# Kernel tuning notes

Measured on AMD Instinct MI355X. Metric: run time of the kernel, lower is better.

Reference implementation:

```python
import jax, jax.numpy as jnp
import numpy as np

B, L, C = 16, 450, 768
MID = 256
K = 8912
TEMP = 0.07
ENT_TEMP = 0.01
EPS_NORM = 1e-12


def _l2norm(v):
    n = jnp.sqrt(jnp.sum(v * v, axis=-1, keepdims=True))
    return v / jnp.maximum(n, EPS_NORM)


def setup_inputs() -> dict:
    key = jax.random.key(0)
    k1, k2, k3, k4 = jax.random.split(key, 4)
    x = jax.random.normal(k1, (B, L, C), dtype=jnp.float32)
    W_down = jax.random.normal(k2, (C, MID), dtype=jnp.float32) * (1.0 / np.sqrt(C))
    b_down = jnp.zeros((MID,), dtype=jnp.float32)
    bound = 1.0 / np.sqrt(MID)
    embedding = jax.random.uniform(k3, (K, MID), dtype=jnp.float32, minval=-bound, maxval=bound)
    return {"x": x, "W_down": W_down, "b_down": b_down, "embedding": embedding}


def reference(x, W_down, b_down, embedding):
    Bx, Lx, Cx = x.shape
    # down projection: [B,L,C] -> [B,L,MID]
    z = jnp.einsum('blc,cm->blm', x, W_down) + b_down
    zf = z.reshape(Bx * Lx, MID)
    zn = _l2norm(zf)                       # [N, MID]
    en = _l2norm(embedding)                # [K, MID]
    # squared euclidean distance on the unit sphere: ||a-b||^2 = 2 - 2 a.b
    d = 2.0 - 2.0 * jnp.einsum('nm,km->nk', zn, en)   # [N, K]
    idx = jnp.argmin(d, axis=1)            # [N]
    # codebook usage (no-grad stats)
    occ = jnp.bincount(idx, length=K)
    code_book_usage = jnp.mean((occ > 0).astype(jnp.float32))
    # soft assignment probs (hard_quant branch)
    logits = -d / TEMP
    probs = jax.nn.softmax(logits, axis=1)
    z_q = en[idx]                          # [N, MID]
    vq_loss = jnp.mean((z_q - jax.lax.stop_gradient(zn)) ** 2)
    commit_loss = jnp.mean((jax.lax.stop_gradient(z_q) - zn) ** 2)
    # straight-through estimator
    z_q_ste = zn + jax.lax.stop_gradient(z_q - zn)
    # entropy loss on affinity = -d at entropy temperature
    fa = -d / ENT_TEMP
    p = jax.nn.softmax(fa, axis=-1)
    lp = jax.nn.log_softmax(fa, axis=-1)
    avg_probs = jnp.mean(p, axis=0)
    avg_entropy = -jnp.sum(avg_probs * jnp.log(avg_probs + 1e-5))
    sample_entropy = -jnp.mean(jnp.sum(p * lp, axis=-1))
    entropy_loss = sample_entropy - avg_entropy
    return (z_q_ste.reshape(Bx, Lx, MID), probs.reshape(Bx, Lx, K),
            code_book_usage, vq_loss, commit_loss, entropy_loss)
```

## Files before the change

kernel.cpp:

```cpp
#include <hip/hip_runtime.h>
#include <stdint.h>

#define N_TOK 7200
#define N_PAD 7232
#define N_PAD_A 7296
#define K_CODE 8912
#define K_PAD 8960
#define N_KT 140
#define NKT128 70
#define NMT128 57
#define MID 256
#define C_DIM 768
#define INV_TEMP (1.0f/0.07f)
#define INV_ETEMP 100.0f
#define MARGIN 0.02f
#define CAND_CAP 64
#define EPS_N 1e-12f

typedef __attribute__((ext_vector_type(8))) short short8;
typedef __attribute__((ext_vector_type(4))) float f32x4;

__device__ __forceinline__ unsigned short f2bf(float f) {
    unsigned u = __float_as_uint(f);
    u += 0x7fffu + ((u >> 16) & 1u);
    return (unsigned short)(u >> 16);
}
__device__ __forceinline__ float bf2f(unsigned short h) {
    return __uint_as_float(((unsigned)h) << 16);
}

__device__ __forceinline__ void gload16(const void* g, void* l) {
    __builtin_amdgcn_global_load_lds(
        (const __attribute__((address_space(1))) unsigned int*)g,
        (__attribute__((address_space(3))) unsigned int*)l,
        16, 0, 0);
}

__global__ void k_prep(const float* __restrict__ emb,
                       float* __restrict__ en, unsigned short* __restrict__ en_h,
                       const float* __restrict__ W,
                       unsigned short* __restrict__ wt_h, unsigned short* __restrict__ wt_l,
                       float* __restrict__ ap_acc, int* __restrict__ used,
                       float* __restrict__ acc4, int* __restrict__ ccnt,
                       unsigned short* __restrict__ zn_h) {
    __shared__ float sb[256];
    int b = blockIdx.x, t = threadIdx.x;
    if (b < K_CODE) {
        float v = emb[b * MID + t];
        sb[t] = v * v; __syncthreads();
        for (int s = 128; s > 0; s >>= 1) { if (t < s) sb[t] += sb[t + s]; __syncthreads(); }
        float nn = sqrtf(sb[0]);
        float o = v / fmaxf(nn, EPS_N);
        en[b * MID + t] = o;
        en_h[b * MID + t] = f2bf(o);
    } else if (b < K_CODE + 768) {
        int i = (b - K_CODE) * 256 + t;
        int c = i / MID, tc = i % MID;
        float v = W[i];
        unsigned short h = f2bf(v);
        unsigned short l = f2bf(v - bf2f(h));
        wt_h[tc * C_DIM + c] = h;
        wt_l[tc * C_DIM + c] = l;
    } else {
        int i = (b - K_CODE - 768) * 256 + t;
        if (i < K_CODE) { ap_acc[i] = 0.f; used[i] = 0; }
        if (i < N_TOK) ccnt[i] = 0;
        if (i < 4) acc4[i] = 0.f;
        for (int j = i; j < (N_PAD_A - N_TOK) * MID; j += 8960) zn_h[(size_t)N_TOK * MID + j] = 0;
        for (int j = i; j < (K_PAD - K_CODE) * MID; j += 8960) en_h[(size_t)K_CODE * MID + j] = 0;
    }
}

__global__ __launch_bounds__(256) void k_zgemm(const float* __restrict__ x,
                                               const unsigned short* __restrict__ wt_h,
                                               const unsigned short* __restrict__ wt_l,
                                               float* __restrict__ zbuf) {
    __shared__ unsigned short ls[4 * 64 * 72];
    unsigned short* xh = ls;
    unsigned short* xl = ls + 64 * 72;
    unsigned short* wh = ls + 2 * 64 * 72;
    unsigned short* wl = ls + 3 * 64 * 72;
    int tid = threadIdx.x;
    int m0 = blockIdx.y * 64;
    int t0 = blockIdx.x * 64;
    int lane = tid & 63, wv = tid >> 6;
    int quad = lane >> 4, l15 = lane & 15;
    int mrow0 = (wv >> 1) * 32, ncol0 = (wv & 1) * 32;
    f32x4 acc[2][2] = {};

    for (int ch = 0; ch < 12; ch++) {
        int c0 = ch * 64;
        for (int it = 0; it < 4; it++) {
            int r = it * 16 + (tid >> 4);
            int cq = tid & 15;
            float4 v = make_float4(0.f, 0.f, 0.f, 0.f);
            int gr = m0 + r;
            if (gr < N_TOK) v = ((const float4*)x)[(size_t)gr * (C_DIM / 4) + (c0 >> 2) + cq];
            unsigned short h0 = f2bf(v.x), h1 = f2bf(v.y), h2 = f2bf(v.z), h3 = f2bf(v.w);
            ushort4 hh = make_ushort4(h0, h1, h2, h3);
            ushort4 ll = make_ushort4(f2bf(v.x - bf2f(h0)), f2bf(v.y - bf2f(h1)),
                                      f2bf(v.z - bf2f(h2)), f2bf(v.w - bf2f(h3)));
            *((ushort4*)&xh[r * 72 + cq * 4]) = hh;
            *((ushort4*)&xl[r * 72 + cq * 4]) = ll;
        }
        for (int it = 0; it < 2; it++) {
            int r = it * 32 + (tid >> 3);
            int cq = tid & 7;
            uint4 vh = ((const uint4*)wt_h)[(size_t)(t0 + r) * (C_DIM / 8) + (c0 >> 3) + cq];
            uint4 vl = ((const uint4*)wt_l)[(size_t)(t0 + r) * (C_DIM / 8) + (c0 >> 3) + cq];
            *((uint4*)&wh[r * 72 + cq * 8]) = vh;
            *((uint4*)&wl[r * 72 + cq * 8]) = vl;
        }
        __syncthreads();
        for (int ks = 0; ks < 2; ks++) {
            int co = ks * 32 + quad * 8;
            short8 ah0 = *((const short8*)&xh[(mrow0 + l15) * 72 + co]);
            short8 ah1 = *((const short8*)&xh[(mrow0 + 16 + l15) * 72 + co]);
            short8 al0 = *((const short8*)&xl[(mrow0 + l15) * 72 + co]);
            short8 al1 = *((const short8*)&xl[(mrow0 + 16 + l15) * 72 + co]);
            short8 bh0 = *((const short8*)&wh[(ncol0 + l15) * 72 + co]);
            short8 bh1 = *((const short8*)&wh[(ncol0 + 16 + l15) * 72 + co]);
            short8 bl0 = *((const short8*)&wl[(ncol0 + l15) * 72 + co]);
            short8 bl1 = *((const short8*)&wl[(ncol0 + 16 + l15) * 72 + co]);
            acc[0][0] = __builtin_amdgcn_mfma_f32_16x16x32_bf16(ah0, bh0, acc[0][0], 0, 0, 0);
            acc[0][1] = __builtin_amdgcn_mfma_f32_16x16x32_bf16(ah0, bh1, acc[0][1], 0, 0, 0);
            acc[1][0] = __builtin_amdgcn_mfma_f32_16x16x32_bf16(ah1, bh0, acc[1][0], 0, 0, 0);
            acc[1][1] = __builtin_amdgcn_mfma_f32_16x16x32_bf16(ah1, bh1, acc[1][1], 0, 0, 0);
            acc[0][0] = __builtin_amdgcn_mfma_f32_16x16x32_bf16(ah0, bl0, acc[0][0], 0, 0, 0);
            acc[0][1] = __builtin_amdgcn_mfma_f32_16x16x32_bf16(ah0, bl1, acc[0][1], 0, 0, 0);
            acc[1][0] = __builtin_amdgcn_mfma_f32_16x16x32_bf16(ah1, bl0, acc[1][0], 0, 0, 0);
            acc[1][1] = __builtin_amdgcn_mfma_f32_16x16x32_bf16(ah1, bl1, acc[1][1], 0, 0, 0);
            acc[0][0] = __builtin_amdgcn_mfma_f32_16x16x32_bf16(al0, bh0, acc[0][0], 0, 0, 0);
            acc[0][1] = __builtin_amdgcn_mfma_f32_16x16x32_bf16(al0, bh1, acc[0][1], 0, 0, 0);
            acc[1][0] = __builtin_amdgcn_mfma_f32_16x16x32_bf16(al1, bh0, acc[1][0], 0, 0, 0);
            acc[1][1] = __builtin_amdgcn_mfma_f32_16x16x32_bf16(al1, bh1, acc[1][1], 0, 0, 0);
        }
        __syncthreads();
    }
    for (int i = 0; i < 2; i++)
        for (int j = 0; j < 2; j++)
            for (int r = 0; r < 4; r++) {
                int gr = m0 + mrow0 + i * 16 + quad * 4 + r;
                int gc = t0 + ncol0 + j * 16 + l15;
                if (gr < N_TOK) zbuf[(size_t)gr * MID + gc] = acc[i][j][r];
            }
}

__global__ void k_znorm(float* __restrict__ zbuf, const float* __restrict__ b_down,
                        unsigned short* __restrict__ zn_h) {
    int n = blockIdx.x, t = threadIdx.x;
    float v = zbuf[(size_t)n * MID + t] + b_down[t];
    __shared__ float sb[256];
    sb[t] = v * v; __syncthreads();
    for (int s = 128; s > 0; s >>= 1) { if (t < s) sb[t] += sb[t + s]; __syncthreads(); }
    float nn = sqrtf(sb[0]);
    float o = v / fmaxf(nn, EPS_N);
    zbuf[(size_t)n * MID + t] = o;
    zn_h[(size_t)n * MID + t] = f2bf(o);
}

__global__ __launch_bounds__(256) void k_dgemm(const unsigned short* __restrict__ zn_h,
                                               const unsigned short* __restrict__ en_h,
                                               float4* __restrict__ part4,
                                               float* __restrict__ out1) {
    __shared__ __align__(16) char lds[32768];
    int tid = threadIdx.x;
    int flat = blockIdx.x * NMT128 + blockIdx.y;
    const int NW = NKT128 * NMT128;
    const int q = NW >> 3, r8 = NW & 7;
    int xcd = flat & 7, sidx = flat >> 3;
    int wg = (xcd < r8 ? xcd * (q + 1) : r8 * (q + 1) + (xcd - r8) * q) + sidx;
    int kt = wg / NMT128, mt = wg - kt * NMT128;
    int m0 = mt * 128, k0 = kt * 128;
    int lane = tid & 63, wv = tid >> 6;
    int quad = lane >> 4, l15 = lane & 15;
    int wr = wv >> 1, wc = wv & 1;
    f32x4 acc[4][4] = {};

    int sr = tid >> 3;
    int scb = (tid & 7) * 16;

    for (int step = 0; step < 4; step++) {
        int cB = step * 128;
        #pragma unroll
        for (int it = 0; it < 4; it++) {
            int r = it * 32 + sr;
            int srcb = scb ^ ((r & 7) << 4);
            gload16((const char*)zn_h + (size_t)(m0 + r) * 512 + cB + srcb,
                    lds + it * 4096 + wv * 1024);
            gload16((const char*)en_h + (size_t)(k0 + r) * 512 + cB + srcb,
                    lds + 16384 + it * 4096 + wv * 1024);
        }
        __syncthreads();
        #pragma unroll
        for (int ks = 0; ks < 2; ks++) {
            short8 a[4], b[4];
            #pragma unroll
            for (int i = 0; i < 4; i++) {
                int ra = wr * 64 + i * 16 + l15;
                int ca = (ks * 64 + quad * 16) ^ ((ra & 7) << 4);
                a[i] = *(const short8*)(lds + ra * 128 + ca);
                int rb = wc * 64 + i * 16 + l15;
                int cb2 = (ks * 64 + quad * 16) ^ ((rb & 7) << 4);
                b[i] = *(const short8*)(lds + 16384 + rb * 128 + cb2);
            }
            #pragma unroll
            for (int i = 0; i < 4; i++)
                #pragma unroll
                for (int j = 0; j < 4; j++)
                    acc[i][j] = __builtin_amdgcn_mfma_f32_16x16x32_bf16(a[i], b[j], acc[i][j], 0, 0, 0);
        }
        __syncthreads();
    }

    int kth = kt * 2 + wc;
    #pragma unroll
    for (int i = 0; i < 4; i++) {
        #pragma unroll
        for (int r = 0; r < 4; r++) {
            int gr = m0 + wr * 64 + i * 16 + quad * 4 + r;
            bool okr = gr < N_TOK;
            float dv[4]; float vmin = 1e30f;
            #pragma unroll
            for (int j = 0; j < 4; j++) {
                int gc = k0 + wc * 64 + j * 16 + l15;
                float d = 2.f - 2.f * acc[i][j][r];
                bool okc = gc < K_CODE;
                dv[j] = okc ? d : 1e30f;
                vmin = fminf(vmin, dv[j]);
                if (okr && okc) out1[(size_t)gr * K_CODE + gc] = d;
            }
            vmin = fminf(vmin, __shfl_xor(vmin, 1));
            vmin = fminf(vmin, __shfl_xor(vmin, 2));
            vmin = fminf(vmin, __shfl_xor(vmin, 4));
            vmin = fminf(vmin, __shfl_xor(vmin, 8));
            float st = 0.f, s1 = 0.f, s2 = 0.f;
            #pragma unroll
            for (int j = 0; j < 4; j++) {
                float dd = vmin - dv[j];
                st += __expf(dd * INV_TEMP);
                float te = dd * INV_ETEMP;
                float e = __expf(te);
                s1 += e; s2 += e * te;
            }
            st += __shfl_xor(st, 1); st += __shfl_xor(st, 2);
            st += __shfl_xor(st, 4); st += __shfl_xor(st, 8);
            s1 += __shfl_xor(s1, 1); s1 += __shfl_xor(s1, 2);
            s1 += __shfl_xor(s1, 4); s1 += __shfl_xor(s1, 8);
            s2 += __shfl_xor(s2, 1); s2 += __shfl_xor(s2, 2);
            s2 += __shfl_xor(s2, 4); s2 += __shfl_xor(s2, 8);
            if (l15 == 0 && okr) {
                part4[(size_t)gr * N_KT + kth] = make_float4(vmin, st, s1, s2);
            }
        }
    }
}

__global__ void k_combine(const float4* __restrict__ part4,
                          float* __restrict__ rs_m, float* __restrict__ rs_ist,
                          float* __restrict__ rs_is1,
                          float* __restrict__ acc4) {
    int sub = threadIdx.x >> 6;
    int row = blockIdx.x * 4 + sub;
    int l = threadIdx.x & 63;
    float4 pv[3];
    float m = 1e30f;
    #pragma unroll
    for (int c = 0; c < 3; c++) {
        int t = l + c * 64;
        pv[c] = (t < N_KT) ? part4[(size_t)row * N_KT + t] : make_float4(1e30f, 0.f, 0.f, 0.f);
        m = fminf(m, pv[c].x);
    }
    #pragma unroll
    for (int s = 1; s < 64; s <<= 1) m = fminf(m, __shfl_xor(m, s));
    float st = 0.f, s1 = 0.f, s2 = 0.f;
    #pragma unroll
    for (int c = 0; c < 3; c++) {
        float mb = pv[c].x;
        int t = l + c * 64;
        if (t < N_KT && mb < 1e29f) {
            float dT = (m - mb) * INV_TEMP;
            st += __expf(dT) * pv[c].y;
            float dE = (m - mb) * INV_ETEMP;
            float e = __expf(dE);
            s1 += e * pv[c].z;
            s2 += e * (pv[c].w + dE * pv[c].z);
        }
    }
    #pragma unroll
    for (int s = 1; s < 64; s <<= 1) {
        st += __shfl_xor(st, s);
        s1 += __shfl_xor(s1, s);
        s2 += __shfl_xor(s2, s);
    }
    if (l == 0) {
        rs_m[row] = m;
        rs_ist[row] = 1.f / st;
        rs_is1[row] = 1.f / s1;
        atomicAdd(&acc4[1], s2 / s1 - __logf(s1));
    }
}

__global__ __launch_bounds__(256) void k_final(float* __restrict__ out1,
                                               const float* __restrict__ rs_m,
                                               const float* __restrict__ rs_ist,
                                               const float* __restrict__ rs_is1,
                                               float* __restrict__ ap_acc,
                                               int* __restrict__ ccnt,
                                               int* __restrict__ cand) {
    __shared__ float lm[128], lt_[128], l1_[128];
    __shared__ float colacc[4 * 256];
    int ct = blockIdx.x, rt = blockIdx.y;
    int r0 = rt * 128, c0 = ct * 256;
    int t = threadIdx.x;
    if (t < 128) {
        int gr = r0 + t;
        bool ok = gr < N_TOK;
        lm[t]  = ok ? rs_m[gr]   : 0.f;
        lt_[t] = ok ? rs_ist[gr] : 0.f;
        l1_[t] = ok ? rs_is1[gr] : 0.f;
    }
    __syncthreads();
    int g = t >> 6;
    int cq = (t & 63) * 4;
    int gc = c0 + cq;
    float ce0 = 0.f, ce1 = 0.f, ce2 = 0.f, ce3 = 0.f;
    if (gc < K_CODE) {
        for (int i = 0; i < 32; i++) {
            int lr = g * 32 + i;
            int gr = r0 + lr;
            if (gr >= N_TOK) break;
            size_t base = (size_t)gr * K_CODE + gc;
            float4 d = *(const float4*)(out1 + base);
            float m_ = lm[lr], tt = lt_[lr], i1 = l1_[lr];
            float thr = m_ + MARGIN;
            ce0 += __expf((m_ - d.x) * INV_ETEMP) * i1;
            ce1 += __expf((m_ - d.y) * INV_ETEMP) * i1;
            ce2 += __expf((m_ - d.z) * INV_ETEMP) * i1;
            ce3 += __expf((m_ - d.w) * INV_ETEMP) * i1;
            float4 p;
            p.x = __expf((m_ - d.x) * INV_TEMP) * tt;
            p.y = __expf((m_ - d.y) * INV_TEMP) * tt;
            p.z = __expf((m_ - d.z) * INV_TEMP) * tt;
            p.w = __expf((m_ - d.w) * INV_TEMP) * tt;
            *((float4*)(out1 + base)) = p;
            if (d.x <= thr) { int pd = atomicAdd(&ccnt[gr], 1); if (pd < CAND_CAP) cand[gr * CAND_CAP + pd] = gc + 0; }
            if (d.y <= thr) { int pd = atomicAdd(&ccnt[gr], 1); if (pd < CAND_CAP) cand[gr * CAND_CAP + pd] = gc + 1; }
            if (d.z <= thr) { int pd = atomicAdd(&ccnt[gr], 1); if (pd < CAND_CAP) cand[gr * CAND_CAP + pd] = gc + 2; }
            if (d.w <= thr) { int pd = atomicAdd(&ccnt[gr], 1); if (pd < CAND_CAP) cand[gr * CAND_CAP + pd] = gc + 3; }
        }
    }
    colacc[g * 256 + cq + 0] = ce0;
    colacc[g * 256 + cq + 1] = ce1;
    colacc[g * 256 + cq + 2] = ce2;
    colacc[g * 256 + cq + 3] = ce3;
    __syncthreads();
    {
        float s = colacc[t] + colacc[256 + t] + colacc[512 + t] + colacc[768 + t];
        int c = c0 + t;
        if (c < K_CODE) atomicAdd(&ap_acc[c], s);
    }
}

__global__ void k_refine(const float* __restrict__ zn, const float* __restrict__ en,
                         const int* __restrict__ ccnt, const int* __restrict__ cand,
                         int* __restrict__ idxb, int* __restrict__ used,
                         float* __restrict__ acc4, float* __restrict__ out0) {
    int n = blockIdx.x * 4 + (threadIdx.x >> 6);
    int lane = threadIdx.x & 63;
    if (n >= N_TOK) return;
    int cnt = ccnt[n];
    if (cnt > CAND_CAP) cnt = CAND_CAP;
    float4 a = ((const float4*)(zn + (size_t)n * MID))[lane];
    float best = 1e30f; int bj = K_CODE;
    for (int c = 0; c < cnt; c++) {
        int code = cand[n * CAND_CAP + c];
        float4 b = ((const float4*)(en + (size_t)code * MID))[lane];
        float s = a.x * b.x + a.y * b.y + a.z * b.z + a.w * b.w;
        #pragma unroll
        for (int off = 1; off < 64; off <<= 1) s += __shfl_xor(s, off);
        float dist = 2.f - 2.f * s;
        if (dist < best || (dist == best && code < bj)) { best = dist; bj = code; }
    }
    float4 b = ((const float4*)(en + (size_t)bj * MID))[lane];
    ((float4*)(out0 + (size_t)n * MID))[lane] = b;
    float dx = b.x - a.x, dy = b.y - a.y, dz = b.z - a.z, dw = b.w - a.w;
    float sq = dx * dx + dy * dy + dz * dz + dw * dw;
    #pragma unroll
    for (int off = 32; off > 0; off >>= 1) sq += __shfl_down(sq, off);
    if (lane == 0) {
        idxb[n] = bj;
        used[bj] = 1;
        atomicAdd(&acc4[0], sq);
    }
}

__global__ void k_scal(const int* __restrict__ used, const float* __restrict__ ap_acc,
                       const float* __restrict__ acc4, float* __restrict__ outs) {
    int t = threadIdx.x;
    float uSum = 0.f, aeSum = 0.f;
    for (int k = t; k < K_CODE; k += 256) {
        uSum += (float)used[k];
        float ap = ap_acc[k] * (1.0f / (float)N_TOK);
        aeSum += ap * __logf(ap + 1e-5f);
    }
    __shared__ float sb[256];
    sb[t] = uSum; __syncthreads();
    for (int s = 128; s > 0; s >>= 1) { if (t < s) sb[t] += sb[t + s]; __syncthreads(); }
    uSum = sb[0];
    __syncthreads(); sb[t] = aeSum; __syncthreads();
    for (int s = 128; s > 0; s >>= 1) { if (t < s) sb[t] += sb[t + s]; __syncthreads(); }
    aeSum = sb[0];
    if (t == 0) {
        outs[0] = uSum / (float)K_CODE;
        float vq = acc4[0] / (float)((size_t)N_TOK * MID);
        outs[1] = vq;
        outs[2] = vq;
        outs[3] = -(acc4[1] / (float)N_TOK) + aeSum;
    }
}

extern "C" void kernel_launch(void* const* d_in, const int* in_sizes, int n_in,
                              void* d_out, int out_size, void* d_ws, size_t ws_size,
                              hipStream_t stream) {
    const float* x   = (const float*)d_in[0];
    const float* W   = (const float*)d_in[1];
    const float* b   = (const float*)d_in[2];
    const float* emb = (const float*)d_in[3];

    float* out  = (float*)d_out;
    float* out0 = out;
    float* out1 = out + (size_t)N_TOK * MID;
    float* outs = out + (size_t)N_TOK * MID + (size_t)N_TOK * K_CODE;

    char* w = (char*)d_ws;
    size_t off = 0;
    auto carve = [&](size_t bytes) { void* p = w + off; off += (bytes + 255) & ~(size_t)255; return p; };
    float*          zn    = (float*)         carve((size_t)N_PAD * MID * 4);
    float*          en    = (float*)         carve((size_t)K_PAD * MID * 4);
    unsigned short* zn_h  = (unsigned short*)carve((size_t)N_PAD_A * MID * 2);
    unsigned short* en_h  = (unsigned short*)carve((size_t)K_PAD * MID * 2);
    unsigned short* wt_h  = (unsigned short*)carve((size_t)MID * C_DIM * 2);
    unsigned short* wt_l  = (unsigned short*)carve((size_t)MID * C_DIM * 2);
    float4*         part4 = (float4*)        carve((size_t)N_TOK * N_KT * 16);
    float*          rs_m  = (float*)         carve((size_t)N_TOK * 4);
    float*          rs_ist= (float*)         carve((size_t)N_TOK * 4);
    float*          rs_is1= (float*)         carve((size_t)N_TOK * 4);
    int*            ccnt  = (int*)           carve((size_t)N_TOK * 4);
    int*            cand  = (int*)           carve((size_t)N_TOK * CAND_CAP * 4);
    int*            idxb  = (int*)           carve((size_t)N_TOK * 4);
    float*          ap_acc= (float*)         carve((size_t)K_CODE * 4);
    int*            used  = (int*)           carve((size_t)K_CODE * 4);
    float*          acc4  = (float*)         carve(16);
    (void)ws_size; (void)in_sizes; (void)n_in; (void)out_size;

    k_prep   <<<K_CODE + 768 + 35, 256, 0, stream>>>(emb, en, en_h, W, wt_h, wt_l,
                                                     ap_acc, used, acc4, ccnt, zn_h);
    k_zgemm  <<<dim3(4, 113), 256, 0, stream>>>(x, wt_h, wt_l, zn);
    k_znorm  <<<N_TOK, 256, 0, stream>>>(zn, b, zn_h);
    k_dgemm  <<<dim3(NKT128, NMT128), 256, 0, stream>>>(zn_h, en_h, part4, out1);
    k_combine<<<N_TOK / 4, 256, 0, stream>>>(part4, rs_m, rs_ist, rs_is1, acc4);
    k_final  <<<dim3(35, 57), 256, 0, stream>>>(out1, rs_m, rs_ist, rs_is1, ap_acc, ccnt, cand);
    k_refine <<<N_TOK / 4, 256, 0, stream>>>(zn, en, ccnt, cand, idxb, used, acc4, out0);
    k_scal   <<<1, 256, 0, stream>>>(used, ap_acc, acc4, outs);
}
```

Measured before the change: 717.2 us.

## Recompute distance GEMM in second pass instead of round-tripping fp32 distances

The distance GEMM now runs twice. The first pass only emits per-tile softmax partials, and the second pass recomputes the distances, stages them in LDS and applies the final softmax, column-entropy and candidate logic directly. This removes writing and then re-reading the full N×K fp32 distance matrix through global memory (about 256 MB of traffic), at the cost of a second bf16 MFMA GEMM and extra LDS use and barriers in the epilogue.

```diff
diff --git a/kernel.cpp b/kernel.cpp
--- a/kernel.cpp
+++ b/kernel.cpp
@@ -159,11 +159,18 @@
     zn_h[(size_t)n * MID + t] = f2bf(o);
 }
 
-__global__ __launch_bounds__(256) void k_dgemm(const unsigned short* __restrict__ zn_h,
+template<int PASS>
+__global__ __launch_bounds__(256) void k_dpass(const unsigned short* __restrict__ zn_h,
                                                const unsigned short* __restrict__ en_h,
                                                float4* __restrict__ part4,
-                                               float* __restrict__ out1) {
-    __shared__ __align__(16) char lds[32768];
+                                               const float* __restrict__ rs_m,
+                                               const float* __restrict__ rs_ist,
+                                               const float* __restrict__ rs_is1,
+                                               float* __restrict__ ap_acc,
+                                               float* __restrict__ out1,
+                                               int* __restrict__ ccnt,
+                                               int* __restrict__ cand) {
+    __shared__ __align__(16) char lds[34048];
     int tid = threadIdx.x;
     int flat = blockIdx.x * NMT128 + blockIdx.y;
     const int NW = NKT128 * NMT128;
@@ -213,45 +220,113 @@
         __syncthreads();
     }
 
-    int kth = kt * 2 + wc;
-    #pragma unroll
-    for (int i = 0; i < 4; i++) {
+    if (PASS == 1) {
+        int kth = kt * 2 + wc;
         #pragma unroll
-        for (int r = 0; r < 4; r++) {
-            int gr = m0 + wr * 64 + i * 16 + quad * 4 + r;
-            bool okr = gr < N_TOK;
-            float dv[4]; float vmin = 1e30f;
+        for (int i = 0; i < 4; i++) {
             #pragma unroll
-            for (int j = 0; j < 4; j++) {
-                int gc = k0 + wc * 64 + j * 16 + l15;
-                float d = 2.f - 2.f * acc[i][j][r];
-                bool okc = gc < K_CODE;
-                dv[j] = okc ? d : 1e30f;
-                vmin = fminf(vmin, dv[j]);
-                if (okr && okc) out1[(size_t)gr * K_CODE + gc] = d;
+            for (int r = 0; r < 4; r++) {
+                float dv[4]; float vmin = 1e30f;
+                #pragma unroll
+                for (int j = 0; j < 4; j++) {
+                    int gc = k0 + wc * 64 + j * 16 + l15;
+                    float d = 2.f - 2.f * acc[i][j][r];
+                    dv[j] = (gc < K_CODE) ? d : 1e30f;
+                    vmin = fminf(vmin, dv[j]);
+                }
+                vmin = fminf(vmin, __shfl_xor(vmin, 1));
+                vmin = fminf(vmin, __shfl_xor(vmin, 2));
+                vmin = fminf(vmin, __shfl_xor(vmin, 4));
+                vmin = fminf(vmin, __shfl_xor(vmin, 8));
+                float st = 0.f, s1 = 0.f, s2 = 0.f;
+                #pragma unroll
+                for (int j = 0; j < 4; j++) {
+                    float dd = vmin - dv[j];
+                    st += __expf(dd * INV_TEMP);
+                    float te = dd * INV_ETEMP;
+                    float e = __expf(te);
+                    s1 += e; s2 += e * te;
+                }
+                st += __shfl_xor(st, 1); st += __shfl_xor(st, 2);
+                st += __shfl_xor(st, 4); st += __shfl_xor(st, 8);
+                s1 += __shfl_xor(s1, 1); s1 += __shfl_xor(s1, 2);
+                s1 += __shfl_xor(s1, 4); s1 += __shfl_xor(s1, 8);
+                s2 += __shfl_xor(s2, 1); s2 += __shfl_xor(s2, 2);
+                s2 += __shfl_xor(s2, 4); s2 += __shfl_xor(s2, 8);
+                if (l15 == 0) {
+                    int gr = m0 + wr * 64 + i * 16 + quad * 4 + r;
+                    if (gr < N_TOK) part4[(size_t)gr * N_KT + kth] = make_float4(vmin, st, s1, s2);
+                }
             }
-            vmin = fminf(vmin, __shfl_xor(vmin, 1));
-            vmin = fminf(vmin, __shfl_xor(vmin, 2));
-            vmin = fminf(vmin, __shfl_xor(vmin, 4));
-            vmin = fminf(vmin, __shfl_xor(vmin, 8));
-            float st = 0.f, s1 = 0.f, s2 = 0.f;
+        }
+    } else {
+        __shared__ float lm[128], lt_[128], l1_[128];
+        __shared__ float colacc[8 * 128];
+        float* sd = (float*)lds;
+        if (tid < 128) {
+            int gr = m0 + tid;
+            bool ok = gr < N_TOK;
+            lm[tid]  = ok ? rs_m[gr]   : 0.f;
+            lt_[tid] = ok ? rs_ist[gr] : 0.f;
+            l1_[tid] = ok ? rs_is1[gr] : 0.f;
+        }
+        int g8 = tid >> 5;
+        int c4 = (tid & 31) * 4;
+        int gc = k0 + c4;
+        bool okc = gc < K_CODE;
+        float ce0 = 0.f, ce1 = 0.f, ce2 = 0.f, ce3 = 0.f;
+        for (int half = 0; half < 2; half++) {
+            if (wr == half) {
+                #pragma unroll
+                for (int i = 0; i < 4; i++)
+                    #pragma unroll
+                    for (int j = 0; j < 4; j++)
+                        #pragma unroll
+                        for (int r = 0; r < 4; r++)
+                            sd[(i * 16 + quad * 4 + r) * 132 + wc * 64 + j * 16 + l15] =
+                                2.f - 2.f * acc[i][j][r];
+            }
+            __syncthreads();
+            if (okc) {
+                #pragma unroll
+                for (int rr = 0; rr < 8; rr++) {
+                    int lr = rr * 8 + g8;
+                    int gr = m0 + half * 64 + lr;
+                    if (gr < N_TOK) {
+                        float4 d = *(const float4*)(sd + lr * 132 + c4);
+                        int sl = half * 64 + lr;
+                        float m_ = lm[sl], tt = lt_[sl], i1 = l1_[sl];
+                        float thr = m_ + MARGIN;
+                        ce0 += __expf((m_ - d.x) * INV_ETEMP) * i1;
+                        ce1 += __expf((m_ - d.y) * INV_ETEMP) * i1;
+                        ce2 += __expf((m_ - d.z) * INV_ETEMP) * i1;
+                        ce3 += __expf((m_ - d.w) * INV_ETEMP) * i1;
+                        float4 p;
+                        p.x = __expf((m_ - d.x) * INV_TEMP) * tt;
+                        p.y = __expf((m_ - d.y) * INV_TEMP) * tt;
+                        p.z = __expf((m_ - d.z) * INV_TEMP) * tt;
+                        p.w = __expf((m_ - d.w) * INV_TEMP) * tt;
+                        *((float4*)(out1 + (size_t)gr * K_CODE + gc)) = p;
+                        if (d.x <= thr) { int pd = atomicAdd(&ccnt[gr], 1); if (pd < CAND_CAP) cand[gr * CAND_CAP + pd] = gc + 0; }
+                        if (d.y <= thr) { int pd = atomicAdd(&ccnt[gr], 1); if (pd < CAND_CAP) cand[gr * CAND_CAP + pd] = gc + 1; }
+                        if (d.z <= thr) { int pd = atomicAdd(&ccnt[gr], 1); if (pd < CAND_CAP) cand[gr * CAND_CAP + pd] = gc + 2; }
+                        if (d.w <= thr) { int pd = atomicAdd(&ccnt[gr], 1); if (pd < CAND_CAP) cand[gr * CAND_CAP + pd] = gc + 3; }
+                    }
+                }
+            }
+            __syncthreads();
+        }
+        colacc[g8 * 128 + c4 + 0] = ce0;
+        colacc[g8 * 128 + c4 + 1] = ce1;
+        colacc[g8 * 128 + c4 + 2] = ce2;
+        colacc[g8 * 128 + c4 + 3] = ce3;
+        __syncthreads();
+        if (tid < 128) {
+            float s = 0.f;
             #pragma unroll
-            for (int j = 0; j < 4; j++) {
-                float dd = vmin - dv[j];
-                st += __expf(dd * INV_TEMP);
-                float te = dd * INV_ETEMP;
-                float e = __expf(te);
-                s1 += e; s2 += e * te;
-            }
-            st += __shfl_xor(st, 1); st += __shfl_xor(st, 2);
-            st += __shfl_xor(st, 4); st += __shfl_xor(st, 8);
-            s1 += __shfl_xor(s1, 1); s1 += __shfl_xor(s1, 2);
-            s1 += __shfl_xor(s1, 4); s1 += __shfl_xor(s1, 8);
-            s2 += __shfl_xor(s2, 1); s2 += __shfl_xor(s2, 2);
-            s2 += __shfl_xor(s2, 4); s2 += __shfl_xor(s2, 8);
-            if (l15 == 0 && okr) {
-                part4[(size_t)gr * N_KT + kth] = make_float4(vmin, st, s1, s2);
-            }
+            for (int g = 0; g < 8; g++) s += colacc[g * 128 + tid];
+            int c = k0 + tid;
+            if (c < K_CODE) atomicAdd(&ap_acc[c], s);
         }
     }
 }
@@ -298,67 +373,6 @@
         rs_ist[row] = 1.f / st;
         rs_is1[row] = 1.f / s1;
         atomicAdd(&acc4[1], s2 / s1 - __logf(s1));
-    }
-}
-
-__global__ __launch_bounds__(256) void k_final(float* __restrict__ out1,
-                                               const float* __restrict__ rs_m,
-                                               const float* __restrict__ rs_ist,
-                                               const float* __restrict__ rs_is1,
-                                               float* __restrict__ ap_acc,
-                                               int* __restrict__ ccnt,
-                                               int* __restrict__ cand) {
-    __shared__ float lm[128], lt_[128], l1_[128];
-    __shared__ float colacc[4 * 256];
-    int ct = blockIdx.x, rt = blockIdx.y;
-    int r0 = rt * 128, c0 = ct * 256;
-    int t = threadIdx.x;
-    if (t < 128) {
-        int gr = r0 + t;
-        bool ok = gr < N_TOK;
-        lm[t]  = ok ? rs_m[gr]   : 0.f;
-        lt_[t] = ok ? rs_ist[gr] : 0.f;
-        l1_[t] = ok ? rs_is1[gr] : 0.f;
-    }
-    __syncthreads();
-    int g = t >> 6;
-    int cq = (t & 63) * 4;
-    int gc = c0 + cq;
-    float ce0 = 0.f, ce1 = 0.f, ce2 = 0.f, ce3 = 0.f;
-    if (gc < K_CODE) {
-        for (int i = 0; i < 32; i++) {
-            int lr = g * 32 + i;
-            int gr = r0 + lr;
-            if (gr >= N_TOK) break;
-            size_t base = (size_t)gr * K_CODE + gc;
-            float4 d = *(const float4*)(out1 + base);
-            float m_ = lm[lr], tt = lt_[lr], i1 = l1_[lr];
-            float thr = m_ + MARGIN;
-            ce0 += __expf((m_ - d.x) * INV_ETEMP) * i1;
-            ce1 += __expf((m_ - d.y) * INV_ETEMP) * i1;
-            ce2 += __expf((m_ - d.z) * INV_ETEMP) * i1;
-            ce3 += __expf((m_ - d.w) * INV_ETEMP) * i1;
-            float4 p;
-            p.x = __expf((m_ - d.x) * INV_TEMP) * tt;
-            p.y = __expf((m_ - d.y) * INV_TEMP) * tt;
-            p.z = __expf((m_ - d.z) * INV_TEMP) * tt;
-            p.w = __expf((m_ - d.w) * INV_TEMP) * tt;
-            *((float4*)(out1 + base)) = p;
-            if (d.x <= thr) { int pd = atomicAdd(&ccnt[gr], 1); if (pd < CAND_CAP) cand[gr * CAND_CAP + pd] = gc + 0; }
-            if (d.y <= thr) { int pd = atomicAdd(&ccnt[gr], 1); if (pd < CAND_CAP) cand[gr * CAND_CAP + pd] = gc + 1; }
-            if (d.z <= thr) { int pd = atomicAdd(&ccnt[gr], 1); if (pd < CAND_CAP) cand[gr * CAND_CAP + pd] = gc + 2; }
-            if (d.w <= thr) { int pd = atomicAdd(&ccnt[gr], 1); if (pd < CAND_CAP) cand[gr * CAND_CAP + pd] = gc + 3; }
-        }
-    }
-    colacc[g * 256 + cq + 0] = ce0;
-    colacc[g * 256 + cq + 1] = ce1;
-    colacc[g * 256 + cq + 2] = ce2;
-    colacc[g * 256 + cq + 3] = ce3;
-    __syncthreads();
-    {
-        float s = colacc[t] + colacc[256 + t] + colacc[512 + t] + colacc[768 + t];
-        int c = c0 + t;
-        if (c < K_CODE) atomicAdd(&ap_acc[c], s);
     }
 }
 
@@ -458,9 +472,9 @@
                                                      ap_acc, used, acc4, ccnt, zn_h);
     k_zgemm  <<<dim3(4, 113), 256, 0, stream>>>(x, wt_h, wt_l, zn);
     k_znorm  <<<N_TOK, 256, 0, stream>>>(zn, b, zn_h);
-    k_dgemm  <<<dim3(NKT128, NMT128), 256, 0, stream>>>(zn_h, en_h, part4, out1);
+    k_dpass<1><<<dim3(NKT128, NMT128), 256, 0, stream>>>(zn_h, en_h, part4, rs_m, rs_ist, rs_is1, ap_acc, out1, ccnt, cand);
     k_combine<<<N_TOK / 4, 256, 0, stream>>>(part4, rs_m, rs_ist, rs_is1, acc4);
-    k_final  <<<dim3(35, 57), 256, 0, stream>>>(out1, rs_m, rs_ist, rs_is1, ap_acc, ccnt, cand);
+    k_dpass<2><<<dim3(NKT128, NMT128), 256, 0, stream>>>(zn_h, en_h, part4, rs_m, rs_ist, rs_is1, ap_acc, out1, ccnt, cand);
     k_refine <<<N_TOK / 4, 256, 0, stream>>>(zn, en, ccnt, cand, idxb, used, acc4, out0);
     k_scal   <<<1, 256, 0, stream>>>(used, ap_acc, acc4, outs);
 }
```

New measurement: 694.4 us. 1.03x faster.
